# Kernel tuning notes

Measured on AMD Instinct MI355X. Metric: run time of the kernel, lower is better.

Reference implementation:

```python
import jax, jax.numpy as jnp
import numpy as np

N = 50000
E = 1000000
WIDTH = 64
DEPTH = 4


def setup_inputs() -> dict:
    key = jax.random.key(0)
    ks = jax.random.split(key, 6)
    x = jax.random.normal(ks[0], (N, 5), dtype=jnp.float32)
    edge_index = jax.random.randint(ks[1], (2, E), 0, N, dtype=jnp.int32)
    edge_attr = jax.random.normal(ks[2], (E, 3), dtype=jnp.float32)
    w1 = jax.random.normal(ks[3], (3, WIDTH), dtype=jnp.float32) / jnp.sqrt(3.0)
    b1 = jnp.zeros((WIDTH,), jnp.float32)
    w2 = jax.random.normal(ks[4], (WIDTH, 1), dtype=jnp.float32) / jnp.sqrt(float(WIDTH))
    b2 = jnp.zeros((1,), jnp.float32)
    root = jax.random.normal(ks[5], (1, 1), dtype=jnp.float32)
    bias = jnp.zeros((1,), jnp.float32)
    return dict(x=x, edge_index=edge_index, edge_attr=edge_attr,
                w1=w1, b1=b1, w2=w2, b2=b2, root=root, bias=bias)


def reference(x, edge_index, edge_attr, w1, b1, w2, b2, root, bias):
    # h: scalar node feature, column 2 of data.x -> [N, 1]
    h = x[:, 2:3]
    src, dst = edge_index[0], edge_index[1]  # messages flow src -> dst

    # Per-edge 1x1 weight from the edge MLP (depends only on edge_attr,
    # identical for all depth iterations since the conv is shared).
    w_e = jax.nn.relu(edge_attr @ w1 + b1) @ w2 + b2  # [E, 1]

    # Mean aggregation: precompute in-degree of each target node.
    deg = jax.ops.segment_sum(jnp.ones((E,), jnp.float32), dst, num_segments=N)
    inv_deg = jnp.where(deg > 0, 1.0 / jnp.maximum(deg, 1.0), 0.0)[:, None]  # [N, 1]

    for _ in range(DEPTH):
        msg = h[src] * w_e                                        # gather + per-edge weight, [E, 1]
        agg = jax.ops.segment_sum(msg, dst, num_segments=N) * inv_deg  # scatter-mean, [N, 1]
        h = jax.nn.relu(agg + h @ root + bias)                    # root transform + bias + ReLU
    return h
```

## Files before the change

### kernel.cpp

```cpp
#include <hip/hip_runtime.h>

#define NN 50000
#define NNP 50176
#define NE 1000000
#define NBK 196
#define ESTRIDE 5632
#define EPC 2048
#define NCH 489

#define EPB 1024
#define PB 977

__global__ __launch_bounds__(512)
void place4(const float* __restrict__ x,
            const float* __restrict__ ea,
            const int* __restrict__ src,
            const int* __restrict__ dst,
            const float* __restrict__ w1,
            const float* __restrict__ b1,
            const float* __restrict__ w2,
            const float* __restrict__ b2,
            uint2* __restrict__ es,
            int* __restrict__ ebase,
            float* __restrict__ hA) {
    __shared__ float sw1[192];
    __shared__ float sb1[64];
    __shared__ float sw2[64];
    __shared__ int hist[NBK];
    __shared__ int part[256];
    __shared__ int lexcl[NBK];
    __shared__ uint2 eLDS[EPC];
    const int t = threadIdx.x;
    const int j = blockIdx.x;
    if (t < 192) sw1[t] = w1[t];
    if (t < 64) { sb1[t] = b1[t]; sw2[t] = w2[t]; }
    if (t < NBK) hist[t] = 0;
    {
        int i = j * 512 + t;
        if (i < NN) hA[i] = x[5 * i + 2];
    }
    __syncthreads();
    const float bz = b2[0];
    const int e0 = j * EPC;
    const int myN = (NE - e0 < EPC) ? (NE - e0) : EPC;

    float ce[4];
    int dd[4], rr[4], ss[4];
#pragma unroll
    for (int k = 0; k < 4; ++k) {
        int p = k * 512 + t;
        dd[k] = -1;
        if (p < myN) {
            int e = e0 + p;
            float a0 = ea[3 * e + 0];
            float a1 = ea[3 * e + 1];
            float a2 = ea[3 * e + 2];
            float c0 = bz, c1 = 0.f, c2 = 0.f, c3 = 0.f;
#pragma unroll
            for (int kk = 0; kk < 64; kk += 4) {
                float h0 = fmaf(a0, sw1[kk+0], fmaf(a1, sw1[64+kk+0], fmaf(a2, sw1[128+kk+0], sb1[kk+0])));
                float h1 = fmaf(a0, sw1[kk+1], fmaf(a1, sw1[64+kk+1], fmaf(a2, sw1[128+kk+1], sb1[kk+1])));
                float h2 = fmaf(a0, sw1[kk+2], fmaf(a1, sw1[64+kk+2], fmaf(a2, sw1[128+kk+2], sb1[kk+2])));
                float h3 = fmaf(a0, sw1[kk+3], fmaf(a1, sw1[64+kk+3], fmaf(a2, sw1[128+kk+3], sb1[kk+3])));
                c0 = fmaf(fmaxf(h0, 0.f), sw2[kk+0], c0);
                c1 = fmaf(fmaxf(h1, 0.f), sw2[kk+1], c1);
                c2 = fmaf(fmaxf(h2, 0.f), sw2[kk+2], c2);
                c3 = fmaf(fmaxf(h3, 0.f), sw2[kk+3], c3);
            }
            ce[k] = (c0 + c1) + (c2 + c3);
            ss[k] = src[e];
            int d = dst[e];
            dd[k] = d;
            rr[k] = atomicAdd(&hist[d >> 8], 1);
        }
    }
    __syncthreads();
    int val = 0;
    if (t < 256) { val = (t < NBK) ? hist[t] : 0; part[t] = val; }
    __syncthreads();
    for (int off = 1; off < 256; off <<= 1) {
        int xv = 0, add = 0;
        if (t < 256) { xv = part[t]; if (t >= off) add = part[t - off]; }
        __syncthreads();
        if (t < 256) part[t] = xv + add;
        __syncthreads();
    }
    if (t < NBK) {
        int excl = part[t] - val;
        lexcl[t] = excl;
        ebase[j * NBK + t] = (excl << 16) | val;
    }
    __syncthreads();
#pragma unroll
    for (int k = 0; k < 4; ++k) {
        if (dd[k] >= 0) {
            int d = dd[k];
            int pos = lexcl[d >> 8] + rr[k];
            eLDS[pos] = make_uint2((unsigned)ss[k] | ((unsigned)(d & 255) << 17),
                                   __float_as_uint(ce[k]));
        }
    }
    __syncthreads();
    for (int p = t; p < myN; p += 512)
        es[e0 + p] = eLDS[p];
}

__global__ __launch_bounds__(1024)
void sortround1(const int* __restrict__ ebase,
                const uint2* __restrict__ es,
                uint2* __restrict__ es2,
                uint2* __restrict__ nodePtr,
                const float* __restrict__ hold,
                float* __restrict__ hnew,
                const float* __restrict__ root,
                const float* __restrict__ bias) {
    __shared__ int cbase[NCH + 1];
    __shared__ int cex[NCH];
    __shared__ int hist[256];
    __shared__ int partc[512];
    __shared__ int part[256];
    __shared__ int cur[256];
    __shared__ float lagg[256];
    const int t = threadIdx.x;
    const int b = blockIdx.x;
    if (t < 256) { hist[t] = 0; lagg[t] = 0.f; }
    int c = 0;
    if (t < NCH) {
        int pk = ebase[t * NBK + b];
        cex[t] = pk >> 16;
        c = pk & 0xFFFF;
    }
    if (t < 512) partc[t] = (t < NCH) ? c : 0;
    __syncthreads();
    for (int off = 1; off < 512; off <<= 1) {
        int xv = 0, add = 0;
        if (t < 512) { xv = partc[t]; if (t >= off) add = partc[t - off]; }
        __syncthreads();
        if (t < 512) partc[t] = xv + add;
        __syncthreads();
    }
    if (t < NCH) cbase[t] = partc[t] - c;
    if (t == 0) cbase[NCH] = partc[NCH - 1];
    __syncthreads();
    const int C = cbase[NCH];

    uint2 v[6]; float hv[6]; bool m[6];
#pragma unroll
    for (int k = 0; k < 6; ++k) {
        int p = k * 1024 + t;
        m[k] = (p < C);
        if (m[k]) {
            int lo = 0, hi = NCH - 1;
            while (lo < hi) { int mid = (lo + hi + 1) >> 1; if (cbase[mid] <= p) lo = mid; else hi = mid - 1; }
            v[k] = es[lo * EPC + cex[lo] + (p - cbase[lo])];
            atomicAdd(&hist[(v[k].x >> 17) & 255], 1);
            hv[k] = hold[v[k].x & 0x1FFFF];
        }
    }
    __syncthreads();
    int val = 0;
    if (t < 256) { val = hist[t]; part[t] = val; }
    __syncthreads();
    for (int off = 1; off < 256; off <<= 1) {
        int xv = 0, add = 0;
        if (t < 256) { xv = part[t]; if (t >= off) add = part[t - off]; }
        __syncthreads();
        if (t < 256) part[t] = xv + add;
        __syncthreads();
    }
    if (t < 256) {
        int excl = part[t] - val;
        cur[t] = excl;
        int ec = (excl < ESTRIDE) ? excl : ESTRIDE;
        nodePtr[b * 256 + t] = make_uint2((unsigned)(b * ESTRIDE + ec), (unsigned)val);
    }
    __syncthreads();
#pragma unroll
    for (int k = 0; k < 6; ++k) {
        if (m[k]) {
            int key = (v[k].x >> 17) & 255;
            int pos = atomicAdd(&cur[key], 1);
            if (pos < ESTRIDE) es2[b * ESTRIDE + pos] = v[k];
            atomicAdd(&lagg[key], hv[k] * __uint_as_float(v[k].y));
        }
    }
    __syncthreads();
    if (t < 256) {
        int node = b * 256 + t;
        if (node < NN) {
            float inv = (val > 0) ? (1.0f / (float)val) : 0.f;
            hnew[node] = fmaxf(fmaf(hold[node], root[0], fmaf(lagg[t], inv, bias[0])), 0.f);
        }
    }
}

__global__ __launch_bounds__(256)
void round_csr(const uint2* __restrict__ nodePtr,
               const uint2* __restrict__ es2,
               const float* __restrict__ hold,
               float* __restrict__ hnew,
               const float* __restrict__ root,
               const float* __restrict__ bias) {
    int g = blockIdx.x * 256 + threadIdx.x;
    int row = g >> 3;
    int sub = g & 7;
    uint2 pk = nodePtr[row];
    int beg = (int)pk.x;
    int len = (int)pk.y;
    bool m0 = (sub      < len), m1 = (sub + 8  < len);
    bool m2 = (sub + 16 < len), m3 = (sub + 24 < len);
    uint2 v0, v1, v2, v3;
    if (m0) v0 = es2[beg + sub];
    if (m1) v1 = es2[beg + sub + 8];
    if (m2) v2 = es2[beg + sub + 16];
    if (m3) v3 = es2[beg + sub + 24];
    float g0 = 0.f, g1 = 0.f, g2 = 0.f, g3 = 0.f;
    if (m0) g0 = hold[v0.x & 0x1FFFF];
    if (m1) g1 = hold[v1.x & 0x1FFFF];
    if (m2) g2 = hold[v2.x & 0x1FFFF];
    if (m3) g3 = hold[v3.x & 0x1FFFF];
    float acc = 0.f;
    if (m0) acc += g0 * __uint_as_float(v0.y);
    if (m1) acc += g1 * __uint_as_float(v1.y);
    if (m2) acc += g2 * __uint_as_float(v2.y);
    if (m3) acc += g3 * __uint_as_float(v3.y);
    for (int k = sub + 32; k < len; k += 8) {
        uint2 v = es2[beg + k];
        acc += hold[v.x & 0x1FFFF] * __uint_as_float(v.y);
    }
    acc += __shfl_xor(acc, 1);
    acc += __shfl_xor(acc, 2);
    acc += __shfl_xor(acc, 4);
    if (sub == 0 && row < NN) {
        float inv = (len > 0) ? (1.0f / (float)len) : 0.f;
        hnew[row] = fmaxf(fmaf(hold[row], root[0], fmaf(acc, inv, bias[0])), 0.f);
    }
}

__global__ void bucket_count(const int* __restrict__ dst, int* __restrict__ bcnt,
                             const float* __restrict__ x, float* __restrict__ h) {
    __shared__ int hist[NBK];
    int t = threadIdx.x;
    if (t < NBK) hist[t] = 0;
    __syncthreads();
    int gid = blockIdx.x * 256 + t;
    if (gid < NN) h[gid] = x[5 * gid + 2];
#pragma unroll
    for (int j = 0; j < 4; ++j) {
        int e = blockIdx.x * EPB + j * 256 + t;
        if (e < NE) atomicAdd(&hist[dst[e] >> 8], 1);
    }
    __syncthreads();
    if (t < NBK && hist[t]) atomicAdd(&bcnt[t], hist[t]);
}

__global__ void bucket_scan(const int* __restrict__ bcnt,
                            int* __restrict__ sBeg,
                            int* __restrict__ cursor,
                            int* __restrict__ sLim) {
    __shared__ int part[256];
    int t = threadIdx.x;
    int v = (t < NBK) ? ((bcnt[t] + 1) & ~1) : 0;
    part[t] = v;
    __syncthreads();
    for (int off = 1; off < 256; off <<= 1) {
        int x = part[t];
        int add = (t >= off) ? part[t - off] : 0;
        __syncthreads();
        part[t] = x + add;
        __syncthreads();
    }
    if (t < NBK) {
        int excl = part[t] - v;
        sBeg[t] = excl;
        cursor[t] = excl;
        sLim[t] = 0x7FFFFFFF;
    }
}

__global__ void place_kernel(const float* __restrict__ ea,
                             const int* __restrict__ src,
                             const int* __restrict__ dst,
                             const float* __restrict__ w1,
                             const float* __restrict__ b1,
                             const float* __restrict__ w2,
                             const float* __restrict__ b2,
                             const int* __restrict__ sLim,
                             int* __restrict__ cursor,
                             uint2* __restrict__ es,
                             int dumpbase) {
    __shared__ float sw1[192];
    __shared__ float sb1[64];
    __shared__ float sw2[64];
    __shared__ float sce[EPB];
    __shared__ int hist[NBK];
    __shared__ int hbase[NBK];
    int t = threadIdx.x;
    if (t < 192) sw1[t] = w1[t];
    if (t < 64) { sb1[t] = b1[t]; sw2[t] = w2[t]; }
    if (t < NBK) hist[t] = 0;
    __syncthreads();

    int r[4], dd[4];
#pragma unroll
    for (int j = 0; j < 4; ++j) {
        int e = blockIdx.x * EPB + j * 256 + t;
        dd[j] = -1;
        if (e < NE) {
            float a0 = ea[3 * e + 0];
            float a1 = ea[3 * e + 1];
            float a2 = ea[3 * e + 2];
            float c0 = b2[0], c1 = 0.f, c2 = 0.f, c3 = 0.f;
#pragma unroll
            for (int k = 0; k < 64; k += 4) {
                float h0 = fmaf(a0, sw1[k+0], fmaf(a1, sw1[64+k+0], fmaf(a2, sw1[128+k+0], sb1[k+0])));
                float h1 = fmaf(a0, sw1[k+1], fmaf(a1, sw1[64+k+1], fmaf(a2, sw1[128+k+1], sb1[k+1])));
                float h2 = fmaf(a0, sw1[k+2], fmaf(a1, sw1[64+k+2], fmaf(a2, sw1[128+k+2], sb1[k+2])));
                float h3 = fmaf(a0, sw1[k+3], fmaf(a1, sw1[64+k+3], fmaf(a2, sw1[128+k+3], sb1[k+3])));
                c0 = fmaf(fmaxf(h0, 0.f), sw2[k+0], c0);
                c1 = fmaf(fmaxf(h1, 0.f), sw2[k+1], c1);
                c2 = fmaf(fmaxf(h2, 0.f), sw2[k+2], c2);
                c3 = fmaf(fmaxf(h3, 0.f), sw2[k+3], c3);
            }
            sce[j * 256 + t] = (c0 + c1) + (c2 + c3);
            int d = dst[e];
            dd[j] = d;
            r[j] = atomicAdd(&hist[d >> 8], 1);
        }
    }
    __syncthreads();
    if (t < NBK) { int hv = hist[t]; if (hv) hbase[t] = atomicAdd(&cursor[t], hv); }
    __syncthreads();
#pragma unroll
    for (int j = 0; j < 4; ++j) {
        int e = blockIdx.x * EPB + j * 256 + t;
        if (e < NE) {
            int d = dd[j];
            int b = d >> 8;
            int pos = hbase[b] + r[j];
            if (pos >= sLim[b]) pos = dumpbase + (t & 63);
            unsigned pack = (unsigned)src[e] | ((unsigned)(d & 255) << 17);
            es[pos] = make_uint2(pack, __float_as_uint(sce[j * 256 + t]));
        }
    }
}

template<int FIRST>
__global__ __launch_bounds__(1024)
void round_fused_fb(const int* __restrict__ sBeg,
                    const int* __restrict__ sEnd,
                    const int* __restrict__ sLim,
                    const uint2* __restrict__ es,
                    const float* __restrict__ hold,
                    float* __restrict__ hnew,
                    float* __restrict__ invdeg,
                    const float* __restrict__ root,
                    const float* __restrict__ bias) {
    __shared__ float lagg[256];
    __shared__ int ldeg[256];
    int t = threadIdx.x;
    int b = blockIdx.x;
    if (t < 256) { lagg[t] = 0.f; if (FIRST) ldeg[t] = 0; }
    __syncthreads();
    int s0 = sBeg[b];
    int s1 = sEnd[b];
    { int cap = sLim[b]; if (s1 > cap) s1 = cap; }
    const uint4* es4 = (const uint4*)es;
    for (int p = s0 + t * 2; p < s1; p += 2048) {
        uint4 v = es4[p >> 1];
        {
            int sidx = v.x & 0x1FFFF;
            int dl = (v.x >> 17) & 255;
            atomicAdd(&lagg[dl], hold[sidx] * __uint_as_float(v.y));
            if (FIRST) atomicAdd(&ldeg[dl], 1);
        }
        if (p + 1 < s1) {
            int sidx = v.z & 0x1FFFF;
            int dl = (v.z >> 17) & 255;
            atomicAdd(&lagg[dl], hold[sidx] * __uint_as_float(v.w));
            if (FIRST) atomicAdd(&ldeg[dl], 1);
        }
    }
    __syncthreads();
    if (t < 256) {
        int node = b * 256 + t;
        if (node < NN) {
            float inv;
            if (FIRST) {
                int d = ldeg[t];
                inv = (d > 0) ? (1.0f / (float)d) : 0.f;
                invdeg[node] = inv;
            } else {
                inv = invdeg[node];
            }
            hnew[node] = fmaxf(fmaf(hold[node], root[0], fmaf(lagg[t], inv, bias[0])), 0.f);
        }
    }
}


extern "C" void kernel_launch(void* const* d_in, const int* in_sizes, int n_in,
                              void* d_out, int out_size, void* d_ws, size_t ws_size,
                              hipStream_t stream) {
    const float* x    = (const float*)d_in[0];
    const int*   ei   = (const int*)d_in[1];
    const float* ea   = (const float*)d_in[2];
    const float* w1   = (const float*)d_in[3];
    const float* b1   = (const float*)d_in[4];
    const float* w2   = (const float*)d_in[5];
    const float* b2   = (const float*)d_in[6];
    const float* root = (const float*)d_in[7];
    const float* bias = (const float*)d_in[8];

    const int* src = ei;
    const int* dst = ei + NE;
    float* out = (float*)d_out;

    const size_t esN  = (size_t)NCH * EPC;
    const size_t es2N = (size_t)NBK * ESTRIDE + 64;
    const size_t needFixed = esN * 8 + es2N * 8
                           + (size_t)(NCH * NBK) * 4
                           + (size_t)NNP * 8
                           + (size_t)NN * 4 * 2;

    if (ws_size >= needFixed) {
        uint2* es      = (uint2*)d_ws;
        uint2* es2     = es + esN;
        int*   ebase   = (int*)(es2 + es2N);
        uint2* nodePtr = (uint2*)(ebase + (size_t)NCH * NBK);
        float* hA      = (float*)(nodePtr + NNP);
        float* hB      = hA + NN;

        place4<<<NCH, 512, 0, stream>>>(x, ea, src, dst, w1, b1, w2, b2,
                                        es, ebase, hA);
        sortround1<<<NBK, 1024, 0, stream>>>(ebase, es, es2, nodePtr,
                                             hA, hB, root, bias);
        const int gR = NNP * 8 / 256;
        round_csr<<<gR, 256, 0, stream>>>(nodePtr, es2, hB, hA, root, bias);
        round_csr<<<gR, 256, 0, stream>>>(nodePtr, es2, hA, hB, root, bias);
        round_csr<<<gR, 256, 0, stream>>>(nodePtr, es2, hB, out, root, bias);
    } else {
        uint2* es     = (uint2*)d_ws;
        int*   bcnt   = (int*)(es + NE + NBK);
        int*   cursor = bcnt + NBK;
        int*   sBeg   = cursor + NBK;
        int*   sLim   = sBeg + NBK;
        float* invdeg = (float*)(sLim + NBK);
        float* hB     = invdeg + NN;
        float* h      = out;

        hipMemsetAsync(bcnt, 0, NBK * 4, stream);
        bucket_count<<<PB, 256, 0, stream>>>(dst, bcnt, x, h);
        bucket_scan<<<1, 256, 0, stream>>>(bcnt, sBeg, cursor, sLim);
        place_kernel<<<PB, 256, 0, stream>>>(ea, src, dst, w1, b1, w2, b2,
                                             sLim, cursor, es, 0);
        round_fused_fb<1><<<NBK, 1024, 0, stream>>>(sBeg, cursor, sLim, es, h,  hB, invdeg, root, bias);
        round_fused_fb<0><<<NBK, 1024, 0, stream>>>(sBeg, cursor, sLim, es, hB, h,  invdeg, root, bias);
        round_fused_fb<0><<<NBK, 1024, 0, stream>>>(sBeg, cursor, sLim, es, h,  hB, invdeg, root, bias);
        round_fused_fb<0><<<NBK, 1024, 0, stream>>>(sBeg, cursor, sLim, es, hB, h,  invdeg, root, bias);
    }
}
```

Measured before the change: 134.5 us.

## Pad per-node CSR rows to even offsets and gather edges as 16-byte pairs

Each node's segment in the sorted edge array now starts at an even offset, which allows round_csr to load two edges per uint4 access. Rows are handled by 4 lanes instead of 8, halving the grid and dropping one shuffle stage. sortround1 also replaces the per-element binary search over chunk bases with a shared lookup table followed by a short linear scan. The padding raises ESTRIDE, so more memory is used and a little more padded traffic is read.

```diff
diff --git a/kernel.cpp b/kernel.cpp
--- a/kernel.cpp
+++ b/kernel.cpp
@@ -4,7 +4,7 @@
 #define NNP 50176
 #define NE 1000000
 #define NBK 196
-#define ESTRIDE 5632
+#define ESTRIDE 5888
 #define EPC 2048
 #define NCH 489
 
@@ -116,6 +116,7 @@
                 const float* __restrict__ bias) {
     __shared__ int cbase[NCH + 1];
     __shared__ int cex[NCH];
+    __shared__ int lut[192];
     __shared__ int hist[256];
     __shared__ int partc[512];
     __shared__ int part[256];
@@ -143,6 +144,13 @@
     if (t == 0) cbase[NCH] = partc[NCH - 1];
     __syncthreads();
     const int C = cbase[NCH];
+    if (t < 192) {
+        int tgt = t * 32;
+        int lo = 0, hi = NCH - 1;
+        while (lo < hi) { int mid = (lo + hi + 1) >> 1; if (cbase[mid] <= tgt) lo = mid; else hi = mid - 1; }
+        lut[t] = lo;
+    }
+    __syncthreads();
 
     uint2 v[6]; float hv[6]; bool m[6];
 #pragma unroll
@@ -150,16 +158,16 @@
         int p = k * 1024 + t;
         m[k] = (p < C);
         if (m[k]) {
-            int lo = 0, hi = NCH - 1;
-            while (lo < hi) { int mid = (lo + hi + 1) >> 1; if (cbase[mid] <= p) lo = mid; else hi = mid - 1; }
+            int lo = lut[p >> 5];
+            while (lo < NCH - 1 && cbase[lo + 1] <= p) ++lo;
             v[k] = es[lo * EPC + cex[lo] + (p - cbase[lo])];
             atomicAdd(&hist[(v[k].x >> 17) & 255], 1);
             hv[k] = hold[v[k].x & 0x1FFFF];
         }
     }
     __syncthreads();
-    int val = 0;
-    if (t < 256) { val = hist[t]; part[t] = val; }
+    int val = 0, ev = 0;
+    if (t < 256) { val = hist[t]; ev = (val + 1) & ~1; part[t] = ev; }
     __syncthreads();
     for (int off = 1; off < 256; off <<= 1) {
         int xv = 0, add = 0;
@@ -169,7 +177,7 @@
         __syncthreads();
     }
     if (t < 256) {
-        int excl = part[t] - val;
+        int excl = part[t] - ev;
         cur[t] = excl;
         int ec = (excl < ESTRIDE) ? excl : ESTRIDE;
         nodePtr[b * 256 + t] = make_uint2((unsigned)(b * ESTRIDE + ec), (unsigned)val);
@@ -202,35 +210,44 @@
                const float* __restrict__ root,
                const float* __restrict__ bias) {
     int g = blockIdx.x * 256 + threadIdx.x;
-    int row = g >> 3;
-    int sub = g & 7;
+    int row = g >> 2;
+    int sub = g & 3;
     uint2 pk = nodePtr[row];
     int beg = (int)pk.x;
     int len = (int)pk.y;
-    bool m0 = (sub      < len), m1 = (sub + 8  < len);
-    bool m2 = (sub + 16 < len), m3 = (sub + 24 < len);
-    uint2 v0, v1, v2, v3;
-    if (m0) v0 = es2[beg + sub];
-    if (m1) v1 = es2[beg + sub + 8];
-    if (m2) v2 = es2[beg + sub + 16];
-    if (m3) v3 = es2[beg + sub + 24];
-    float g0 = 0.f, g1 = 0.f, g2 = 0.f, g3 = 0.f;
-    if (m0) g0 = hold[v0.x & 0x1FFFF];
-    if (m1) g1 = hold[v1.x & 0x1FFFF];
-    if (m2) g2 = hold[v2.x & 0x1FFFF];
-    if (m3) g3 = hold[v3.x & 0x1FFFF];
+    const uint4* e4 = (const uint4*)es2;
+    const int b4 = (beg >> 1) + sub;
+    const int r0 = 2 * sub;
+    bool n0 = (r0      < len), n0b = (r0 + 1  < len);
+    bool n1 = (r0 + 8  < len), n1b = (r0 + 9  < len);
+    bool n2 = (r0 + 16 < len), n2b = (r0 + 17 < len);
+    uint4 u0, u1, u2;
+    if (n0) u0 = e4[b4];
+    if (n1) u1 = e4[b4 + 4];
+    if (n2) u2 = e4[b4 + 8];
+    float ga = 0.f, gb = 0.f, gc = 0.f, gd = 0.f, ge = 0.f, gf = 0.f;
+    if (n0)  ga = hold[u0.x & 0x1FFFF];
+    if (n0b) gb = hold[u0.z & 0x1FFFF];
+    if (n1)  gc = hold[u1.x & 0x1FFFF];
+    if (n1b) gd = hold[u1.z & 0x1FFFF];
+    if (n2)  ge = hold[u2.x & 0x1FFFF];
+    if (n2b) gf = hold[u2.z & 0x1FFFF];
     float acc = 0.f;
-    if (m0) acc += g0 * __uint_as_float(v0.y);
-    if (m1) acc += g1 * __uint_as_float(v1.y);
-    if (m2) acc += g2 * __uint_as_float(v2.y);
-    if (m3) acc += g3 * __uint_as_float(v3.y);
-    for (int k = sub + 32; k < len; k += 8) {
-        uint2 v = es2[beg + k];
-        acc += hold[v.x & 0x1FFFF] * __uint_as_float(v.y);
+    if (n0)  acc += ga * __uint_as_float(u0.y);
+    if (n0b) acc += gb * __uint_as_float(u0.w);
+    if (n1)  acc += gc * __uint_as_float(u1.y);
+    if (n1b) acc += gd * __uint_as_float(u1.w);
+    if (n2)  acc += ge * __uint_as_float(u2.y);
+    if (n2b) acc += gf * __uint_as_float(u2.w);
+    for (int i = b4 + 12; ; i += 4) {
+        int rel = 2 * (i - (beg >> 1));
+        if (rel >= len) break;
+        uint4 u = e4[i];
+        acc += hold[u.x & 0x1FFFF] * __uint_as_float(u.y);
+        if (rel + 1 < len) acc += hold[u.z & 0x1FFFF] * __uint_as_float(u.w);
     }
     acc += __shfl_xor(acc, 1);
     acc += __shfl_xor(acc, 2);
-    acc += __shfl_xor(acc, 4);
     if (sub == 0 && row < NN) {
         float inv = (len > 0) ? (1.0f / (float)len) : 0.f;
         hnew[row] = fmaxf(fmaf(hold[row], root[0], fmaf(acc, inv, bias[0])), 0.f);
@@ -435,7 +452,7 @@
                                         es, ebase, hA);
         sortround1<<<NBK, 1024, 0, stream>>>(ebase, es, es2, nodePtr,
                                              hA, hB, root, bias);
-        const int gR = NNP * 8 / 256;
+        const int gR = NNP * 4 / 256;
         round_csr<<<gR, 256, 0, stream>>>(nodePtr, es2, hB, hA, root, bias);
         round_csr<<<gR, 256, 0, stream>>>(nodePtr, es2, hA, hB, root, bias);
         round_csr<<<gR, 256, 0, stream>>>(nodePtr, es2, hB, out, root, bias);
```

After: 139.1 us. 1.03x slower.
